# Optimization experiments

Hardware: AMD Instinct MI355X
Metric: run time of the kernel (lower is better)

## Reference

```python
import jax, jax.numpy as jnp
import numpy as np

N_PMTS = 12
N_TICKS = 550
BIN_SIGMA = 0.1
GAUSS_NORM = 1.0 / (BIN_SIGMA * 2.5066282746)
B, N_DEP, K = 8, 64, 512  # batch, depositions/event, electron slot cap per deposition


def setup_inputs() -> dict:
    key = jax.random.key(0)
    ks = jax.random.split(key, 10)
    # energy depositions [B, N, 4] = x, y, z, E(MeV)
    xy = jax.random.normal(ks[0], (B, N_DEP, 2), dtype=jnp.float32) * 5.0
    z = jax.random.uniform(ks[1], (B, N_DEP, 1), dtype=jnp.float32, minval=50.0, maxval=500.0)
    # E ~ 0.0115 MeV -> n = E*1e6/22.4 ~ up to ~513 electrons, capped at K
    E = jax.random.uniform(ks[2], (B, N_DEP, 1), dtype=jnp.float32, minval=0.002, maxval=0.0115)
    energy_depositions = jnp.concatenate([xy, z, E], axis=-1)
    return {
        "energy_depositions": energy_depositions,
        "e_draws": jax.random.normal(ks[3], (B, N_DEP), dtype=jnp.float32),
        "diff_draws": jax.random.normal(ks[4], (B, N_DEP, K, 3), dtype=jnp.float32),
        "unif_draws": jax.random.uniform(ks[5], (B, N_DEP, K), dtype=jnp.float32),
        "W1": jax.random.normal(ks[6], (2, 28), dtype=jnp.float32) * (1.0 / np.sqrt(2.0)),
        "b1": jnp.zeros((28,), dtype=jnp.float32),
        "W2": jax.random.normal(ks[7], (28, 12), dtype=jnp.float32) * (1.0 / np.sqrt(28.0)),
        "b2": jnp.zeros((12,), dtype=jnp.float32),
        "diffusion_scale": jnp.array([1.0, 1.0, 0.25], dtype=jnp.float32),
        "pmt_response_scale": jnp.ones((12,), dtype=jnp.float32),
        "lifetime": jnp.float32(25.0),
    }


def reference(energy_depositions, e_draws, diff_draws, unif_draws,
              W1, b1, W2, b2, diffusion_scale, pmt_response_scale, lifetime):
    dt = energy_depositions.dtype
    pos = energy_depositions[..., :3]            # [B,N,3]
    E = energy_depositions[..., 3]               # [B,N]
    # generate_electrons: n = E*1e6/22.4, sigma = sqrt(0.15 n)
    n = E * 1000.0 * 1000.0 / 22.4
    sigma = jnp.sqrt(0.15 * n)
    n_elec = jnp.clip((sigma * e_draws + n).astype(jnp.int32), 0, K)  # [B,N]
    slot_mask = jnp.arange(K)[None, None, :] < n_elec[..., None]       # [B,N,K]
    # diffuse_electrons: scale^2 * draw * sqrt(z) + position
    sqrt_z = jnp.sqrt(pos[..., 2])                                     # [B,N]
    elec = (diffusion_scale ** 2) * diff_draws * sqrt_z[..., None, None] + pos[:, :, None, :]  # [B,N,K,3]
    z_e = elec[..., 2]                                                 # [B,N,K]
    # apply_lifetime: accept with prob 1 - exp(-z/lifetime)
    prob = 1.0 - jnp.exp(-z_e / lifetime)
    mask = (slot_mask & (prob > unif_draws)).astype(dt)                # [B,N,K]
    # PMT response MLP on xy, scaled
    xy_e = elec[..., :2]
    h = jax.nn.sigmoid(xy_e @ W1 + b1)
    pmt = jax.nn.sigmoid(h @ W2 + b2) * (pmt_response_scale ** 2)      # [B,N,K,12]
    pmt = pmt * mask[..., None]
    # gaussian tick histogram over 550 ticks centered at 0.5..549.5
    ticks = jnp.arange(N_TICKS, dtype=dt) + 0.5
    g = GAUSS_NORM * jnp.exp(-((ticks - z_e[..., None]) ** 2) / BIN_SIGMA)  # [B,N,K,550]
    # sum over all electrons of the event: [B, 12, 550]
    return jnp.einsum('bnkp,bnkt->bpt', pmt, g)
```

## Files before the change

### kernel.cpp

```cpp
#include <hip/hip_runtime.h>
#include <hip/hip_fp16.h>

#define NB   8
#define NDEP 64
#define KK   512
#define NP   12
#define NT   550

static __device__ __forceinline__ float sigmoidf_fast(float x) {
    return 1.0f / (1.0f + __expf(-x));
}
static __device__ __forceinline__ unsigned packh2(float a, float b) {
    __half2 h = __floats2half2_rn(a, b);
    return __builtin_bit_cast(unsigned, h);
}
static __device__ __forceinline__ float2 unpackh2(unsigned u) {
    return __half22float2(__builtin_bit_cast(__half2, u));
}

template<int S>
static __device__ __forceinline__ void gather_reduce(
    const unsigned* __restrict__ wl, int lane, int t_lo, int b,
    float* __restrict__ out)
{
    constexpr int W = 64 / S;
    const int tw  = lane & (W - 1);
    const int sub = lane / W;
    const float tc = (float)(t_lo + tw) + 0.5f;

    float acc[NP];
    #pragma unroll
    for (int p = 0; p < NP; ++p) acc[p] = 0.0f;

    #pragma unroll 4
    for (int i = 0; i < W; ++i) {
        const int k = sub * W + i;
        const int o = k * 8 + ((k >> 4) << 2);
        const uint4 r0 = *(const uint4*)&wl[o];
        const uint4 r1 = *(const uint4*)&wl[o + 4];
        const float ez = __builtin_bit_cast(float, r1.z);
        const float d  = tc - ez;
        const float g  = exp2f(-14.426950408889634f * d * d);
        const float2 u0 = unpackh2(r0.x), u1 = unpackh2(r0.y);
        const float2 u2 = unpackh2(r0.z), u3 = unpackh2(r0.w);
        const float2 u4 = unpackh2(r1.x), u5 = unpackh2(r1.y);
        acc[0] = fmaf(u0.x, g, acc[0]);  acc[1]  = fmaf(u0.y, g, acc[1]);
        acc[2] = fmaf(u1.x, g, acc[2]);  acc[3]  = fmaf(u1.y, g, acc[3]);
        acc[4] = fmaf(u2.x, g, acc[4]);  acc[5]  = fmaf(u2.y, g, acc[5]);
        acc[6] = fmaf(u3.x, g, acc[6]);  acc[7]  = fmaf(u3.y, g, acc[7]);
        acc[8] = fmaf(u4.x, g, acc[8]);  acc[9]  = fmaf(u4.y, g, acc[9]);
        acc[10] = fmaf(u5.x, g, acc[10]); acc[11] = fmaf(u5.y, g, acc[11]);
    }

    #pragma unroll
    for (int msk = W; msk < 64; msk <<= 1) {
        #pragma unroll
        for (int p = 0; p < NP; ++p) acc[p] += __shfl_xor(acc[p], msk);
    }

    if (lane < W) {
        float* ob = out + ((size_t)b * NP) * NT + (t_lo + tw);
        #pragma unroll
        for (int p = 0; p < NP; ++p) atomicAdd(&ob[p * NT], acc[p]);
    }
}

__global__ __launch_bounds__(256) void next_sim_wave(
    const float* __restrict__ ed,
    const float* __restrict__ edraw,
    const float* __restrict__ ddraw,
    const float* __restrict__ udraw,
    const float* __restrict__ W1, const float* __restrict__ b1,
    const float* __restrict__ W2, const float* __restrict__ b2,
    const float* __restrict__ dscale, const float* __restrict__ pscale,
    const float* __restrict__ life,
    float* __restrict__ out)
{
    __shared__ unsigned lds[4][544];

    const int tid  = threadIdx.x;
    const int lane = tid & 63;
    const int wid  = tid >> 6;
    const int bid  = blockIdx.x;
    const int bn   = bid >> 1;
    const int g    = ((bid & 1) << 2) | wid;
    const int b    = bn >> 6;

    const float4 dep  = ((const float4*)ed)[bn];
    const float nval  = dep.w * (1000000.0f / 22.4f);
    const float sigma = sqrtf(0.15f * nval);
    int ne = (int)(sigma * edraw[bn] + nval);
    ne = min(max(ne, 0), KK);
    const int k0 = g << 6;
    if (k0 >= ne) return;

    const float sqz     = sqrtf(dep.z);
    const float invLife = 1.0f / life[0];
    const float dS0 = dscale[0] * dscale[0];
    const float dS1 = dscale[1] * dscale[1];
    const float dS2 = dscale[2] * dscale[2];

    const int k = k0 + lane;
    const float* dd = ddraw + ((size_t)bn * KK + k) * 3;
    const float d0 = dd[0], d1 = dd[1], d2 = dd[2];
    const float ez = fmaf(dS2 * d2, sqz, dep.z);
    const float ex = fmaf(dS0 * d0, sqz, dep.x);
    const float ey = fmaf(dS1 * d1, sqz, dep.y);
    const float prob = 1.0f - __expf(-ez * invLife);
    const float m = ((k < ne) && (prob > udraw[(size_t)bn * KK + k])) ? 1.0f : 0.0f;

    float pm[NP];
    #pragma unroll
    for (int p = 0; p < NP; ++p) pm[p] = b2[p];
    #pragma unroll 4
    for (int j = 0; j < 28; ++j) {
        const float hj = sigmoidf_fast(fmaf(W1[j], ex, fmaf(W1[28 + j], ey, b1[j])));
        #pragma unroll
        for (int p = 0; p < NP; ++p) pm[p] = fmaf(hj, W2[j * NP + p], pm[p]);
    }
    const float gm = 3.9894228040143274f * m;
    float q[NP];
    #pragma unroll
    for (int p = 0; p < NP; ++p)
        q[p] = pscale[p] * pscale[p] * gm * sigmoidf_fast(pm[p]);

    unsigned* wl = lds[wid];
    const int off = lane * 8 + ((lane >> 4) << 2);
    uint4 r0, r1;
    r0.x = packh2(q[0], q[1]);   r0.y = packh2(q[2],  q[3]);
    r0.z = packh2(q[4], q[5]);   r0.w = packh2(q[6],  q[7]);
    r1.x = packh2(q[8], q[9]);   r1.y = packh2(q[10], q[11]);
    r1.z = __builtin_bit_cast(unsigned, ez);  r1.w = 0u;
    *(uint4*)&wl[off]     = r0;
    *(uint4*)&wl[off + 4] = r1;

    float ezmin = ez, ezmax = ez;
    #pragma unroll
    for (int msk = 1; msk < 64; msk <<= 1) {
        ezmin = fminf(ezmin, __shfl_xor(ezmin, msk));
        ezmax = fmaxf(ezmax, __shfl_xor(ezmax, msk));
    }
    const int fmin = (int)floorf(ezmin);
    const int fmax = (int)floorf(ezmax);
    const int need = fmax - fmin + 7;

    if (need <= 16) {
        const int t_lo = min(max(fmin - 3, 0), NT - 16);
        gather_reduce<4>(wl, lane, t_lo, b, out);
    } else {
        const int t_lo = min(max(fmin - 3, 0), NT - 32);
        gather_reduce<2>(wl, lane, t_lo, b, out);
    }
}

extern "C" void kernel_launch(void* const* d_in, const int* in_sizes, int n_in,
                              void* d_out, int out_size, void* d_ws, size_t ws_size,
                              hipStream_t stream) {
    const float* ed     = (const float*)d_in[0];
    const float* edraw  = (const float*)d_in[1];
    const float* ddraw  = (const float*)d_in[2];
    const float* udraw  = (const float*)d_in[3];
    const float* W1     = (const float*)d_in[4];
    const float* b1     = (const float*)d_in[5];
    const float* W2     = (const float*)d_in[6];
    const float* b2     = (const float*)d_in[7];
    const float* dscale = (const float*)d_in[8];
    const float* pscale = (const float*)d_in[9];
    const float* life   = (const float*)d_in[10];
    float* out = (float*)d_out;

    hipMemsetAsync(d_out, 0, (size_t)out_size * sizeof(float), stream);
    next_sim_wave<<<NB * NDEP * 2, 256, 0, stream>>>(
        ed, edraw, ddraw, udraw, W1, b1, W2, b2, dscale, pscale, life, out);
}
```

Before: 22.97 us.

## Precompute packed MLP weights in an init kernel and use half2 FMA for the second layer

A small init kernel replaces the memset. It zeroes the output and writes prescaled W1/b1 (multiplied by log2 e), W2/b2 packed as half2, and the squared pscale times the Gaussian norm into the workspace. The main kernel then runs the hidden-to-output MLP layer with packed half2 FMAs and uses hardware reciprocal and exp2 for the sigmoids. The per-electron LDS records are widened to fp32 to avoid half unpacking in the gather loop. The cost is twice the LDS footprint and reduced precision in the accumulation of the second MLP layer.

```diff
diff --git a/kernel.cpp b/kernel.cpp
--- a/kernel.cpp
+++ b/kernel.cpp
@@ -6,21 +6,51 @@
 #define KK   512
 #define NP   12
 #define NT   550
-
-static __device__ __forceinline__ float sigmoidf_fast(float x) {
-    return 1.0f / (1.0f + __expf(-x));
+#define L2E  1.4426950408889634f
+
+
+static __device__ __forceinline__ float fast_rcp(float x) {
+    return __builtin_amdgcn_rcpf(x);
 }
 static __device__ __forceinline__ unsigned packh2(float a, float b) {
     __half2 h = __floats2half2_rn(a, b);
     return __builtin_bit_cast(unsigned, h);
 }
-static __device__ __forceinline__ float2 unpackh2(unsigned u) {
-    return __half22float2(__builtin_bit_cast(__half2, u));
+
+__global__ __launch_bounds__(256) void init_kernel(
+    const float* __restrict__ W1, const float* __restrict__ b1,
+    const float* __restrict__ W2, const float* __restrict__ b2,
+    const float* __restrict__ pscale,
+    float* __restrict__ ws, float* __restrict__ out, int out_size)
+{
+    const int idx = blockIdx.x * 256 + threadIdx.x;
+    for (int i = idx; i < out_size; i += gridDim.x * 256) out[i] = 0.0f;
+
+    if (blockIdx.x == 0) {
+        const int t = threadIdx.x;
+        if (t < 28) {
+            ws[t]      = W1[t]      * L2E;
+            ws[28 + t] = W1[28 + t] * L2E;
+            ws[56 + t] = b1[t]      * L2E;
+        }
+        if (t >= 64 && t < 232) {
+            const int e = t - 64, j = e / 6, c = e - j * 6;
+            ((unsigned*)(ws + 84))[e] = packh2(W2[j * NP + 2 * c], W2[j * NP + 2 * c + 1]);
+        }
+        if (t >= 232 && t < 238) {
+            const int c = t - 232;
+            ((unsigned*)(ws + 252))[c] = packh2(b2[2 * c], b2[2 * c + 1]);
+        }
+        if (t >= 238 && t < 250) {
+            const int p = t - 238;
+            ws[258 + p] = pscale[p] * pscale[p] * 3.9894228040143274f;
+        }
+    }
 }
 
 template<int S>
 static __device__ __forceinline__ void gather_reduce(
-    const unsigned* __restrict__ wl, int lane, int t_lo, int b,
+    const float* __restrict__ wl, int lane, int t_lo, int b,
     float* __restrict__ out)
 {
     constexpr int W = 64 / S;
@@ -35,21 +65,19 @@
     #pragma unroll 4
     for (int i = 0; i < W; ++i) {
         const int k = sub * W + i;
-        const int o = k * 8 + ((k >> 4) << 2);
-        const uint4 r0 = *(const uint4*)&wl[o];
-        const uint4 r1 = *(const uint4*)&wl[o + 4];
-        const float ez = __builtin_bit_cast(float, r1.z);
-        const float d  = tc - ez;
-        const float g  = exp2f(-14.426950408889634f * d * d);
-        const float2 u0 = unpackh2(r0.x), u1 = unpackh2(r0.y);
-        const float2 u2 = unpackh2(r0.z), u3 = unpackh2(r0.w);
-        const float2 u4 = unpackh2(r1.x), u5 = unpackh2(r1.y);
-        acc[0] = fmaf(u0.x, g, acc[0]);  acc[1]  = fmaf(u0.y, g, acc[1]);
-        acc[2] = fmaf(u1.x, g, acc[2]);  acc[3]  = fmaf(u1.y, g, acc[3]);
-        acc[4] = fmaf(u2.x, g, acc[4]);  acc[5]  = fmaf(u2.y, g, acc[5]);
-        acc[6] = fmaf(u3.x, g, acc[6]);  acc[7]  = fmaf(u3.y, g, acc[7]);
-        acc[8] = fmaf(u4.x, g, acc[8]);  acc[9]  = fmaf(u4.y, g, acc[9]);
-        acc[10] = fmaf(u5.x, g, acc[10]); acc[11] = fmaf(u5.y, g, acc[11]);
+        const int o = (k << 4) + ((k >> 4) << 2);
+        const float4 r0 = *(const float4*)&wl[o];
+        const float4 r1 = *(const float4*)&wl[o + 4];
+        const float4 r2 = *(const float4*)&wl[o + 8];
+        const float ez  = wl[o + 12];
+        const float d   = tc - ez;
+        const float g   = exp2f(-14.426950408889634f * d * d);
+        acc[0]  = fmaf(r0.x, g, acc[0]);  acc[1]  = fmaf(r0.y, g, acc[1]);
+        acc[2]  = fmaf(r0.z, g, acc[2]);  acc[3]  = fmaf(r0.w, g, acc[3]);
+        acc[4]  = fmaf(r1.x, g, acc[4]);  acc[5]  = fmaf(r1.y, g, acc[5]);
+        acc[6]  = fmaf(r1.z, g, acc[6]);  acc[7]  = fmaf(r1.w, g, acc[7]);
+        acc[8]  = fmaf(r2.x, g, acc[8]);  acc[9]  = fmaf(r2.y, g, acc[9]);
+        acc[10] = fmaf(r2.z, g, acc[10]); acc[11] = fmaf(r2.w, g, acc[11]);
     }
 
     #pragma unroll
@@ -70,13 +98,11 @@
     const float* __restrict__ edraw,
     const float* __restrict__ ddraw,
     const float* __restrict__ udraw,
-    const float* __restrict__ W1, const float* __restrict__ b1,
-    const float* __restrict__ W2, const float* __restrict__ b2,
-    const float* __restrict__ dscale, const float* __restrict__ pscale,
-    const float* __restrict__ life,
+    const float* __restrict__ wst,
+    const float* __restrict__ dscale, const float* __restrict__ life,
     float* __restrict__ out)
 {
-    __shared__ unsigned lds[4][544];
+    __shared__ float lds[4][1040];
 
     const int tid  = threadIdx.x;
     const int lane = tid & 63;
@@ -95,7 +121,7 @@
     if (k0 >= ne) return;
 
     const float sqz     = sqrtf(dep.z);
-    const float invLife = 1.0f / life[0];
+    const float invLife = fast_rcp(life[0]);
     const float dS0 = dscale[0] * dscale[0];
     const float dS1 = dscale[1] * dscale[1];
     const float dS2 = dscale[2] * dscale[2];
@@ -109,30 +135,47 @@
     const float prob = 1.0f - __expf(-ez * invLife);
     const float m = ((k < ne) && (prob > udraw[(size_t)bn * KK + k])) ? 1.0f : 0.0f;
 
-    float pm[NP];
-    #pragma unroll
-    for (int p = 0; p < NP; ++p) pm[p] = b2[p];
+    const float*   w1a  = wst;
+    const float*   w1b  = wst + 28;
+    const float*   b1s  = wst + 56;
+    const __half2* w2pk = (const __half2*)(wst + 84);
+    const __half2* b2pk = (const __half2*)(wst + 252);
+    const float*   qtab = wst + 258;
+
+    __half2 pa0 = b2pk[0], pa1 = b2pk[1], pa2 = b2pk[2];
+    __half2 pa3 = b2pk[3], pa4 = b2pk[4], pa5 = b2pk[5];
     #pragma unroll 4
     for (int j = 0; j < 28; ++j) {
-        const float hj = sigmoidf_fast(fmaf(W1[j], ex, fmaf(W1[28 + j], ey, b1[j])));
-        #pragma unroll
-        for (int p = 0; p < NP; ++p) pm[p] = fmaf(hj, W2[j * NP + p], pm[p]);
-    }
-    const float gm = 3.9894228040143274f * m;
+        const float lg  = fmaf(w1a[j], ex, fmaf(w1b[j], ey, b1s[j]));
+        const float hjf = fast_rcp(1.0f + exp2f(-lg));
+        const __half2 h2 = __float2half2_rn(hjf);
+        pa0 = __hfma2(h2, w2pk[j * 6 + 0], pa0);
+        pa1 = __hfma2(h2, w2pk[j * 6 + 1], pa1);
+        pa2 = __hfma2(h2, w2pk[j * 6 + 2], pa2);
+        pa3 = __hfma2(h2, w2pk[j * 6 + 3], pa3);
+        pa4 = __hfma2(h2, w2pk[j * 6 + 4], pa4);
+        pa5 = __hfma2(h2, w2pk[j * 6 + 5], pa5);
+    }
+    float pm[NP];
+    { float2 f;
+      f = __half22float2(pa0); pm[0] = f.x; pm[1] = f.y;
+      f = __half22float2(pa1); pm[2] = f.x; pm[3] = f.y;
+      f = __half22float2(pa2); pm[4] = f.x; pm[5] = f.y;
+      f = __half22float2(pa3); pm[6] = f.x; pm[7] = f.y;
+      f = __half22float2(pa4); pm[8] = f.x; pm[9] = f.y;
+      f = __half22float2(pa5); pm[10] = f.x; pm[11] = f.y; }
+
     float q[NP];
     #pragma unroll
     for (int p = 0; p < NP; ++p)
-        q[p] = pscale[p] * pscale[p] * gm * sigmoidf_fast(pm[p]);
-
-    unsigned* wl = lds[wid];
-    const int off = lane * 8 + ((lane >> 4) << 2);
-    uint4 r0, r1;
-    r0.x = packh2(q[0], q[1]);   r0.y = packh2(q[2],  q[3]);
-    r0.z = packh2(q[4], q[5]);   r0.w = packh2(q[6],  q[7]);
-    r1.x = packh2(q[8], q[9]);   r1.y = packh2(q[10], q[11]);
-    r1.z = __builtin_bit_cast(unsigned, ez);  r1.w = 0u;
-    *(uint4*)&wl[off]     = r0;
-    *(uint4*)&wl[off + 4] = r1;
+        q[p] = qtab[p] * m * fast_rcp(1.0f + exp2f(-pm[p] * L2E));
+
+    float* wl = lds[wid];
+    const int off = (lane << 4) + ((lane >> 4) << 2);
+    *(float4*)&wl[off]     = make_float4(q[0], q[1],  q[2],  q[3]);
+    *(float4*)&wl[off + 4] = make_float4(q[4], q[5],  q[6],  q[7]);
+    *(float4*)&wl[off + 8] = make_float4(q[8], q[9],  q[10], q[11]);
+    wl[off + 12] = ez;
 
     float ezmin = ez, ezmax = ez;
     #pragma unroll
@@ -167,9 +210,10 @@
     const float* dscale = (const float*)d_in[8];
     const float* pscale = (const float*)d_in[9];
     const float* life   = (const float*)d_in[10];
+    float* ws  = (float*)d_ws;
     float* out = (float*)d_out;
 
-    hipMemsetAsync(d_out, 0, (size_t)out_size * sizeof(float), stream);
+    init_kernel<<<64, 256, 0, stream>>>(W1, b1, W2, b2, pscale, ws, out, out_size);
     next_sim_wave<<<NB * NDEP * 2, 256, 0, stream>>>(
-        ed, edraw, ddraw, udraw, W1, b1, W2, b2, dscale, pscale, life, out);
-}
+        ed, edraw, ddraw, udraw, ws, dscale, life, out);
+}
```

Measured after the change: 20.66 us. 1.11x faster.

## Restructure into output-tile owned blocks, dropping atomics and memset

Applied to the files above, without the earlier changes.

The kernel now launches one block per (batch, 16-tick chunk). Each block scans all depositions, skips those whose z is far from its chunk, and recomputes electron diffusion and the MLP for the electron groups that overlap. Partial sums are reduced in LDS and written directly, which removes the global atomics and the separate memset launch. LDS storage switches from packed fp16 to fp32. The trade-off is redundant MLP work whenever a group overlaps several chunks, plus a serial loop over depositions inside each block.

```diff
diff --git a/kernel.cpp b/kernel.cpp
--- a/kernel.cpp
+++ b/kernel.cpp
@@ -1,71 +1,18 @@
 #include <hip/hip_runtime.h>
-#include <hip/hip_fp16.h>
 
 #define NB   8
 #define NDEP 64
 #define KK   512
 #define NP   12
 #define NT   550
+#define CH   16
+#define NCH  35
+#define L2E  1.4426950408889634f
+#define GN   3.9894228040143274f
 
-static __device__ __forceinline__ float sigmoidf_fast(float x) {
-    return 1.0f / (1.0f + __expf(-x));
-}
-static __device__ __forceinline__ unsigned packh2(float a, float b) {
-    __half2 h = __floats2half2_rn(a, b);
-    return __builtin_bit_cast(unsigned, h);
-}
-static __device__ __forceinline__ float2 unpackh2(unsigned u) {
-    return __half22float2(__builtin_bit_cast(__half2, u));
-}
+static __device__ __forceinline__ float frcp(float x) { return __builtin_amdgcn_rcpf(x); }
 
-template<int S>
-static __device__ __forceinline__ void gather_reduce(
-    const unsigned* __restrict__ wl, int lane, int t_lo, int b,
-    float* __restrict__ out)
-{
-    constexpr int W = 64 / S;
-    const int tw  = lane & (W - 1);
-    const int sub = lane / W;
-    const float tc = (float)(t_lo + tw) + 0.5f;
-
-    float acc[NP];
-    #pragma unroll
-    for (int p = 0; p < NP; ++p) acc[p] = 0.0f;
-
-    #pragma unroll 4
-    for (int i = 0; i < W; ++i) {
-        const int k = sub * W + i;
-        const int o = k * 8 + ((k >> 4) << 2);
-        const uint4 r0 = *(const uint4*)&wl[o];
-        const uint4 r1 = *(const uint4*)&wl[o + 4];
-        const float ez = __builtin_bit_cast(float, r1.z);
-        const float d  = tc - ez;
-        const float g  = exp2f(-14.426950408889634f * d * d);
-        const float2 u0 = unpackh2(r0.x), u1 = unpackh2(r0.y);
-        const float2 u2 = unpackh2(r0.z), u3 = unpackh2(r0.w);
-        const float2 u4 = unpackh2(r1.x), u5 = unpackh2(r1.y);
-        acc[0] = fmaf(u0.x, g, acc[0]);  acc[1]  = fmaf(u0.y, g, acc[1]);
-        acc[2] = fmaf(u1.x, g, acc[2]);  acc[3]  = fmaf(u1.y, g, acc[3]);
-        acc[4] = fmaf(u2.x, g, acc[4]);  acc[5]  = fmaf(u2.y, g, acc[5]);
-        acc[6] = fmaf(u3.x, g, acc[6]);  acc[7]  = fmaf(u3.y, g, acc[7]);
-        acc[8] = fmaf(u4.x, g, acc[8]);  acc[9]  = fmaf(u4.y, g, acc[9]);
-        acc[10] = fmaf(u5.x, g, acc[10]); acc[11] = fmaf(u5.y, g, acc[11]);
-    }
-
-    #pragma unroll
-    for (int msk = W; msk < 64; msk <<= 1) {
-        #pragma unroll
-        for (int p = 0; p < NP; ++p) acc[p] += __shfl_xor(acc[p], msk);
-    }
-
-    if (lane < W) {
-        float* ob = out + ((size_t)b * NP) * NT + (t_lo + tw);
-        #pragma unroll
-        for (int p = 0; p < NP; ++p) atomicAdd(&ob[p * NT], acc[p]);
-    }
-}
-
-__global__ __launch_bounds__(256) void next_sim_wave(
+__global__ __launch_bounds__(512) void next_sim_onepass(
     const float* __restrict__ ed,
     const float* __restrict__ edraw,
     const float* __restrict__ ddraw,
@@ -76,80 +23,143 @@
     const float* __restrict__ life,
     float* __restrict__ out)
 {
-    __shared__ unsigned lds[4][544];
+    __shared__ float rows[8][1040];
+    __shared__ float part[8][CH * NP];
+    __shared__ float xArr[NDEP], yArr[NDEP], zArr[NDEP];
+    __shared__ int   neArr[NDEP];
 
     const int tid  = threadIdx.x;
     const int lane = tid & 63;
     const int wid  = tid >> 6;
-    const int bid  = blockIdx.x;
-    const int bn   = bid >> 1;
-    const int g    = ((bid & 1) << 2) | wid;
-    const int b    = bn >> 6;
+    const int b    = blockIdx.x / NCH;
+    const int c    = blockIdx.x % NCH;
+    const int t0i  = c * CH;
+    const float t0 = (float)t0i;
 
-    const float4 dep  = ((const float4*)ed)[bn];
-    const float nval  = dep.w * (1000000.0f / 22.4f);
-    const float sigma = sqrtf(0.15f * nval);
-    int ne = (int)(sigma * edraw[bn] + nval);
-    ne = min(max(ne, 0), KK);
-    const int k0 = g << 6;
-    if (k0 >= ne) return;
+    if (tid < NDEP) {
+        const float4 dep = ((const float4*)ed)[b * NDEP + tid];
+        const float nval = dep.w * (1000000.0f / 22.4f);
+        const float sg   = sqrtf(0.15f * nval);
+        int ne = (int)(sg * edraw[b * NDEP + tid] + nval);
+        neArr[tid] = min(max(ne, 0), KK);
+        xArr[tid] = dep.x; yArr[tid] = dep.y; zArr[tid] = dep.z;
+    }
+    __syncthreads();
 
-    const float sqz     = sqrtf(dep.z);
-    const float invLife = 1.0f / life[0];
+    const float cLife = -frcp(life[0]) * L2E;
     const float dS0 = dscale[0] * dscale[0];
     const float dS1 = dscale[1] * dscale[1];
     const float dS2 = dscale[2] * dscale[2];
+    float qt[NP];
+    #pragma unroll
+    for (int p = 0; p < NP; ++p) qt[p] = pscale[p] * pscale[p] * GN;
 
-    const int k = k0 + lane;
-    const float* dd = ddraw + ((size_t)bn * KK + k) * 3;
-    const float d0 = dd[0], d1 = dd[1], d2 = dd[2];
-    const float ez = fmaf(dS2 * d2, sqz, dep.z);
-    const float ex = fmaf(dS0 * d0, sqz, dep.x);
-    const float ey = fmaf(dS1 * d1, sqz, dep.y);
-    const float prob = 1.0f - __expf(-ez * invLife);
-    const float m = ((k < ne) && (prob > udraw[(size_t)bn * KK + k])) ? 1.0f : 0.0f;
+    const int   tw  = lane & 15;
+    const int   sub = lane >> 4;
+    const float tc  = t0 + (float)tw + 0.5f;
+    float acc[NP];
+    #pragma unroll
+    for (int p = 0; p < NP; ++p) acc[p] = 0.0f;
 
-    float pm[NP];
+    float* wl = rows[wid];
+    const int off = (lane << 4) + ((lane >> 4) << 2);
+
+    int jc = 0;
+    for (int n = 0; n < NDEP; ++n) {
+        const int nen = neArr[n];
+        if (nen == 0) continue;
+        const float zn = zArr[n];
+        if (zn < t0 - 16.0f || zn > t0 + 32.0f) continue;
+        const int nkg = (nen + 63) >> 6;
+        const float sqz = sqrtf(zn);
+
+        for (int kg = 0; kg < nkg; ++kg) {
+            const bool mine = ((jc & 7) == wid); ++jc;
+            if (!mine) continue;
+
+            const int k = (kg << 6) + lane;
+            const size_t base = (size_t)(b * NDEP + n) * KK + k;
+            const float* dd = ddraw + base * 3;
+            const float d0 = dd[0], d1 = dd[1], d2 = dd[2];
+            const float u  = udraw[base];
+
+            const float ez = fmaf(dS2 * d2, sqz, zn);
+
+            float ezmin = ez, ezmax = ez;
+            #pragma unroll
+            for (int msk = 1; msk < 64; msk <<= 1) {
+                ezmin = fminf(ezmin, __shfl_xor(ezmin, msk));
+                ezmax = fmaxf(ezmax, __shfl_xor(ezmax, msk));
+            }
+            if (ezmax < t0 - 2.6f || ezmin > t0 + 18.6f) continue;
+
+            const float prob = 1.0f - exp2f(ez * cLife);
+            const float m = ((k < nen) && (prob > u)) ? 1.0f : 0.0f;
+            const float ex = fmaf(dS0 * d0, sqz, xArr[n]);
+            const float ey = fmaf(dS1 * d1, sqz, yArr[n]);
+
+            float pm[NP];
+            #pragma unroll
+            for (int p = 0; p < NP; ++p) pm[p] = b2[p];
+            #pragma unroll 4
+            for (int j = 0; j < 28; ++j) {
+                const float lg = fmaf(W1[j], ex, fmaf(W1[28 + j], ey, b1[j]));
+                const float hj = frcp(1.0f + exp2f(-lg * L2E));
+                #pragma unroll
+                for (int p = 0; p < NP; ++p) pm[p] = fmaf(hj, W2[j * NP + p], pm[p]);
+            }
+            float q[NP];
+            #pragma unroll
+            for (int p = 0; p < NP; ++p)
+                q[p] = qt[p] * m * frcp(1.0f + exp2f(-pm[p] * L2E));
+
+            *(float4*)&wl[off]     = make_float4(q[0], q[1],  q[2],  q[3]);
+            *(float4*)&wl[off + 4] = make_float4(q[4], q[5],  q[6],  q[7]);
+            *(float4*)&wl[off + 8] = make_float4(q[8], q[9],  q[10], q[11]);
+            wl[off + 12] = ez;
+
+            #pragma unroll 4
+            for (int i = 0; i < 16; ++i) {
+                const int kk = (sub << 4) + i;
+                const int o  = (kk << 4) + ((kk >> 4) << 2);
+                const float4 r0 = *(const float4*)&wl[o];
+                const float4 r1 = *(const float4*)&wl[o + 4];
+                const float4 r2 = *(const float4*)&wl[o + 8];
+                const float ezr = wl[o + 12];
+                const float d   = tc - ezr;
+                const float g   = exp2f(-14.426950408889634f * d * d);
+                acc[0]  = fmaf(r0.x, g, acc[0]);  acc[1]  = fmaf(r0.y, g, acc[1]);
+                acc[2]  = fmaf(r0.z, g, acc[2]);  acc[3]  = fmaf(r0.w, g, acc[3]);
+                acc[4]  = fmaf(r1.x, g, acc[4]);  acc[5]  = fmaf(r1.y, g, acc[5]);
+                acc[6]  = fmaf(r1.z, g, acc[6]);  acc[7]  = fmaf(r1.w, g, acc[7]);
+                acc[8]  = fmaf(r2.x, g, acc[8]);  acc[9]  = fmaf(r2.y, g, acc[9]);
+                acc[10] = fmaf(r2.z, g, acc[10]); acc[11] = fmaf(r2.w, g, acc[11]);
+            }
+        }
+    }
+
     #pragma unroll
-    for (int p = 0; p < NP; ++p) pm[p] = b2[p];
-    #pragma unroll 4
-    for (int j = 0; j < 28; ++j) {
-        const float hj = sigmoidf_fast(fmaf(W1[j], ex, fmaf(W1[28 + j], ey, b1[j])));
+    for (int msk = 16; msk < 64; msk <<= 1) {
         #pragma unroll
-        for (int p = 0; p < NP; ++p) pm[p] = fmaf(hj, W2[j * NP + p], pm[p]);
+        for (int p = 0; p < NP; ++p) acc[p] += __shfl_xor(acc[p], msk);
     }
-    const float gm = 3.9894228040143274f * m;
-    float q[NP];
-    #pragma unroll
-    for (int p = 0; p < NP; ++p)
-        q[p] = pscale[p] * pscale[p] * gm * sigmoidf_fast(pm[p]);
+    if (lane < 16) {
+        float* pp = &part[wid][lane * NP];
+        *(float4*)&pp[0] = make_float4(acc[0], acc[1],  acc[2],  acc[3]);
+        *(float4*)&pp[4] = make_float4(acc[4], acc[5],  acc[6],  acc[7]);
+        *(float4*)&pp[8] = make_float4(acc[8], acc[9],  acc[10], acc[11]);
+    }
+    __syncthreads();
 
-    unsigned* wl = lds[wid];
-    const int off = lane * 8 + ((lane >> 4) << 2);
-    uint4 r0, r1;
-    r0.x = packh2(q[0], q[1]);   r0.y = packh2(q[2],  q[3]);
-    r0.z = packh2(q[4], q[5]);   r0.w = packh2(q[6],  q[7]);
-    r1.x = packh2(q[8], q[9]);   r1.y = packh2(q[10], q[11]);
-    r1.z = __builtin_bit_cast(unsigned, ez);  r1.w = 0u;
-    *(uint4*)&wl[off]     = r0;
-    *(uint4*)&wl[off + 4] = r1;
-
-    float ezmin = ez, ezmax = ez;
-    #pragma unroll
-    for (int msk = 1; msk < 64; msk <<= 1) {
-        ezmin = fminf(ezmin, __shfl_xor(ezmin, msk));
-        ezmax = fmaxf(ezmax, __shfl_xor(ezmax, msk));
-    }
-    const int fmin = (int)floorf(ezmin);
-    const int fmax = (int)floorf(ezmax);
-    const int need = fmax - fmin + 7;
-
-    if (need <= 16) {
-        const int t_lo = min(max(fmin - 3, 0), NT - 16);
-        gather_reduce<4>(wl, lane, t_lo, b, out);
-    } else {
-        const int t_lo = min(max(fmin - 3, 0), NT - 32);
-        gather_reduce<2>(wl, lane, t_lo, b, out);
+    if (tid < CH * NP) {
+        const int p   = tid >> 4;
+        const int twi = tid & 15;
+        float s = 0.0f;
+        #pragma unroll
+        for (int w = 0; w < 8; ++w) s += part[w][twi * NP + p];
+        const int t = t0i + twi;
+        if (t < NT)
+            out[(size_t)(b * NP + p) * NT + t] = s;
     }
 }
 
@@ -169,7 +179,6 @@
     const float* life   = (const float*)d_in[10];
     float* out = (float*)d_out;
 
-    hipMemsetAsync(d_out, 0, (size_t)out_size * sizeof(float), stream);
-    next_sim_wave<<<NB * NDEP * 2, 256, 0, stream>>>(
+    next_sim_onepass<<<NB * NCH, 512, 0, stream>>>(
         ed, edraw, ddraw, udraw, W1, b1, W2, b2, dscale, pscale, life, out);
 }
```

New measurement: 47.17 us. +105.4%, slower.
